# Kernel optimization log

Hardware: AMD Instinct MI355X
Metric: run time of the kernel (lower is better)

The kernel has to match this reference:

```python
import jax, jax.numpy as jnp
import numpy as np

HEADS = 12
D_MODEL = 768
D_TOKEN = D_MODEL // HEADS


def setup_inputs() -> dict:
    key = jax.random.key(0)
    ks = jax.random.split(key, 11)
    B, S, D = 2, 4096, D_MODEL
    scale = 1.0 / np.sqrt(D)
    return {
        "q": jax.random.normal(ks[0], (B, S, D), jnp.float32),
        "k": jax.random.normal(ks[1], (B, S, D), jnp.float32),
        "v": jax.random.normal(ks[2], (B, S, D), jnp.float32),
        "Wq": jax.random.normal(ks[3], (D, D), jnp.float32) * scale,
        "bq": jnp.zeros((D,), jnp.float32),
        "Wk": jax.random.normal(ks[4], (D, D), jnp.float32) * scale,
        "bk": jnp.zeros((D,), jnp.float32),
        "Wv": jax.random.normal(ks[5], (D, D), jnp.float32) * scale,
        "bv": jnp.zeros((D,), jnp.float32),
        "Wo": jax.random.normal(ks[6], (D, D), jnp.float32) * scale,
        "bo": jnp.zeros((D,), jnp.float32),
    }


def reference(q, k, v, Wq, bq, Wk, bk, Wv, bv, Wo, bo):
    B, S, D = q.shape
    H, Dh = HEADS, D_TOKEN
    # Linear projections (torch Linear: x @ W.T + b), split into heads: [B,H,S,Dh]
    qh = (q @ Wq.T + bq).reshape(B, S, H, Dh).transpose(0, 2, 1, 3)
    kh = (k @ Wk.T + bk).reshape(B, S, H, Dh).transpose(0, 2, 1, 3)
    vh = (v @ Wv.T + bv).reshape(B, S, H, Dh).transpose(0, 2, 1, 3)
    # Scaled dot-product attention (full O(S^2) scores, as the original does)
    scores = jnp.einsum("bhqd,bhkd->bhqk", qh, kh) / jnp.sqrt(
        jnp.asarray(Dh, qh.dtype))
    attn = jax.nn.softmax(scores, axis=-1)
    ctx = jnp.einsum("bhqk,bhkd->bhqd", attn, vh)
    ctx = ctx.transpose(0, 2, 1, 3).reshape(B, S, D)
    return ctx @ Wo.T + bo
```

## Files before the change

### kernel.cpp

```cpp
#include <hip/hip_runtime.h>


typedef __attribute__((ext_vector_type(4))) float f32x4;
typedef __attribute__((ext_vector_type(16))) float f32x16;
typedef __attribute__((ext_vector_type(8))) __bf16 bf16x8;
typedef __attribute__((ext_vector_type(2))) int i32x2;
typedef __attribute__((ext_vector_type(4))) unsigned u32x4;
using u16 = unsigned short;
using u32 = unsigned;

__device__ __forceinline__ u16 f2bf(float x) {
  __bf16 h = (__bf16)x;
  return __builtin_bit_cast(u16, h);
}
__device__ __forceinline__ u32 pk2(float lo, float hi) {
  u32 r;
  asm("v_cvt_pk_bf16_f32 %0, %1, %2" : "=v"(r) : "v"(lo), "v"(hi));
  return r;
}
__device__ __forceinline__ void gload16(u16* ldsDst, const u16* gSrc) {
  __builtin_amdgcn_global_load_lds(
      (const __attribute__((address_space(1))) void*)gSrc,
      (__attribute__((address_space(3))) void*)ldsDst, 16, 0, 0);
}
__device__ __forceinline__ f32x4 mfma16(bf16x8 a, bf16x8 b, f32x4 c) {
  return __builtin_amdgcn_mfma_f32_16x16x32_bf16(a, b, c, 0, 0, 0);
}
__device__ __forceinline__ f32x16 mfma32(bf16x8 a, bf16x8 b, f32x16 c) {
  return __builtin_amdgcn_mfma_f32_32x32x16_bf16(a, b, c, 0, 0, 0);
}
__device__ __forceinline__ bf16x8 ld8(const u16* p) { return *(const bf16x8*)p; }

__global__ void cvt_hi(const float4* __restrict__ in0, u16* o0,
                       const float4* __restrict__ in1, u16* o1,
                       const float4* __restrict__ in2, u16* o2,
                       const float4* __restrict__ in3, u16* o3, int n4) {
  const float4* in = in0; u16* o = o0;
  if (blockIdx.y == 1) { in = in1; o = o1; }
  else if (blockIdx.y == 2) { in = in2; o = o2; }
  else if (blockIdx.y == 3) { in = in3; o = o3; }
  const int stride = gridDim.x * blockDim.x;
  for (int i = blockIdx.x * blockDim.x + threadIdx.x; i < n4; i += stride) {
    float4 x = in[i];
    *(ushort4*)&o[i * 4] = make_ushort4(f2bf(x.x), f2bf(x.y), f2bf(x.z), f2bf(x.w));
  }
}

__global__ __launch_bounds__(256, 2) void gemm_qkv(
    const u16* __restrict__ Aq, const u16* __restrict__ Ak, const u16* __restrict__ Av,
    const u16* __restrict__ wq, const u16* __restrict__ wk, const u16* __restrict__ wv,
    const float* __restrict__ bq, const float* __restrict__ bk,
    const float* __restrict__ bv,
    u16* __restrict__ oq, u16* __restrict__ ok, u16* __restrict__ ov,
    float qscale) {
  constexpr int K = 768;
  constexpr int BUF = 8192;
  __shared__ u16 lds[2 * BUF];
  const int z = blockIdx.z;
  const u16* A = (z == 0) ? Aq : (z == 1) ? Ak : Av;
  const u16* Bh = (z == 0) ? wq : (z == 1) ? wk : wv;
  const float* bias = (z == 0) ? bq : (z == 1) ? bk : bv;
  u16* C = (z == 0) ? oq : (z == 1) ? ok : ov;
  const float scale = (z == 0) ? qscale : 1.f;
  const bool vmode = (z == 2);

  const int tid = threadIdx.x, lane = tid & 63, w = tid >> 6;
  const int wr = w >> 1, wc = w & 1;
  const int g = lane >> 4, la = lane & 15;
  const int m0 = blockIdx.x * 128, n0 = blockIdx.y * 128;

  f32x4 acc[4][4] = {};

  auto stage = [&](int buf, int kt) {
    const int k0 = kt * 32;
#pragma unroll
    for (int j = 0; j < 2; ++j) {
      const int t = w * 2 + j;
      const int s = t * 64 + lane;
      const int sr = s >> 3, ph = s & 7, ch = ph ^ (sr & 7);
      const int row = sr * 2 + (ch >> 2), c = ch & 3;
      const int gofs = k0 + c * 8;
      u16* base = &lds[buf * BUF];
      gload16(base + t * 512, A + (size_t)(m0 + row) * K + gofs);
      gload16(base + 4096 + t * 512, Bh + (size_t)(n0 + row) * K + gofs);
    }
  };
  auto rdfrag = [&](const u16* base, int row, int c) -> bf16x8 {
    const int sr = row >> 1;
    const int ph = (((row & 1) << 2) | c) ^ (sr & 7);
    return ld8(base + sr * 64 + ph * 8);
  };

  stage(0, 0);
  __syncthreads();
  constexpr int nk = K / 32;
  int cur = 0;
  for (int kt = 0; kt < nk; ++kt) {
    if (kt + 1 < nk) stage(cur ^ 1, kt + 1);
    const u16* bA = &lds[cur * BUF];
    bf16x8 aH[4], bH[4];
#pragma unroll
    for (int mi = 0; mi < 4; ++mi) aH[mi] = rdfrag(bA, wr * 64 + mi * 16 + la, g);
#pragma unroll
    for (int ni = 0; ni < 4; ++ni) bH[ni] = rdfrag(bA + 4096, wc * 64 + ni * 16 + la, g);
#pragma unroll
    for (int mi = 0; mi < 4; ++mi)
#pragma unroll
      for (int ni = 0; ni < 4; ++ni)
        acc[mi][ni] = mfma16(aH[mi], bH[ni], acc[mi][ni]);
    __syncthreads();
    cur ^= 1;
  }

#pragma unroll
  for (int mi = 0; mi < 4; ++mi) {
    const int mbase = m0 + wr * 64 + mi * 16 + g * 4;
#pragma unroll
    for (int ni = 0; ni < 4; ++ni) {
      const int n = n0 + wc * 64 + ni * 16 + la;
      const float bv_ = bias[n];
#pragma unroll
      for (int r = 0; r < 4; ++r) {
        const int m = mbase + r;
        const float y = (acc[mi][ni][r] + bv_) * scale;
        const int bb = m >> 12, s = m & 4095, hh = n >> 6, dh = n & 63;
        if (!vmode)
          C[((size_t)(bb * 12 + hh) * 4096 + s) * 64 + dh] = f2bf(y);
        else
          C[((size_t)(bb * 12 + hh) * 64 + dh) * 4096 + s] = f2bf(y);
      }
    }
  }
}

__global__ __launch_bounds__(256, 2) void gemm_out(
    const u16* __restrict__ A, const u16* __restrict__ Bh,
    const float* __restrict__ bias, float* __restrict__ Cf) {
  constexpr int K = 768, N = 768;
  constexpr int BUF = 8192;
  __shared__ u16 lds[2 * BUF];
  const int tid = threadIdx.x, lane = tid & 63, w = tid >> 6;
  const int wr = w >> 1, wc = w & 1;
  const int g = lane >> 4, la = lane & 15;
  const int m0 = blockIdx.x * 128, n0 = blockIdx.y * 128;

  f32x4 acc[4][4] = {};

  auto stage = [&](int buf, int kt) {
    const int k0 = kt * 32;
#pragma unroll
    for (int j = 0; j < 2; ++j) {
      const int t = w * 2 + j;
      const int s = t * 64 + lane;
      const int sr = s >> 3, ph = s & 7, ch = ph ^ (sr & 7);
      const int row = sr * 2 + (ch >> 2), c = ch & 3;
      const int gofs = k0 + c * 8;
      u16* base = &lds[buf * BUF];
      gload16(base + t * 512, A + (size_t)(m0 + row) * K + gofs);
      gload16(base + 4096 + t * 512, Bh + (size_t)(n0 + row) * K + gofs);
    }
  };
  auto rdfrag = [&](const u16* base, int row, int c) -> bf16x8 {
    const int sr = row >> 1;
    const int ph = (((row & 1) << 2) | c) ^ (sr & 7);
    return ld8(base + sr * 64 + ph * 8);
  };

  stage(0, 0);
  __syncthreads();
  constexpr int nk = K / 32;
  int cur = 0;
  for (int kt = 0; kt < nk; ++kt) {
    if (kt + 1 < nk) stage(cur ^ 1, kt + 1);
    const u16* bA = &lds[cur * BUF];
    bf16x8 aH[4], bH[4];
#pragma unroll
    for (int mi = 0; mi < 4; ++mi) aH[mi] = rdfrag(bA, wr * 64 + mi * 16 + la, g);
#pragma unroll
    for (int ni = 0; ni < 4; ++ni) bH[ni] = rdfrag(bA + 4096, wc * 64 + ni * 16 + la, g);
#pragma unroll
    for (int mi = 0; mi < 4; ++mi)
#pragma unroll
      for (int ni = 0; ni < 4; ++ni)
        acc[mi][ni] = mfma16(aH[mi], bH[ni], acc[mi][ni]);
    __syncthreads();
    cur ^= 1;
  }

#pragma unroll
  for (int mi = 0; mi < 4; ++mi) {
    const int mbase = m0 + wr * 64 + mi * 16 + g * 4;
#pragma unroll
    for (int ni = 0; ni < 4; ++ni) {
      const int n = n0 + wc * 64 + ni * 16 + la;
      const float bv_ = bias[n];
#pragma unroll
      for (int r = 0; r < 4; ++r)
        Cf[(size_t)(mbase + r) * N + n] = acc[mi][ni][r] + bv_;
    }
  }
}

__global__ __launch_bounds__(256, 3) void flash_attn(
    const u16* __restrict__ Q, const u16* __restrict__ Kt,
    const u16* __restrict__ Vt, u16* __restrict__ ctx) {
  __shared__ u16 lds[2 * 8192];
  const int tid = threadIdx.x, lane = tid & 63, w = tid >> 6;
  const int l5 = lane & 31, hi = lane >> 5;
  const int bh = blockIdx.y, b = bh / 12, h = bh % 12;
  const int q0 = blockIdx.x * 128 + w * 32;
  const size_t kbase = (size_t)bh * 4096 * 64;
  const size_t vbase = (size_t)bh * 64 * 4096;

  bf16x8 aQ[4];
#pragma unroll
  for (int ks = 0; ks < 4; ++ks)
    aQ[ks] = ld8(Q + kbase + (size_t)(q0 + l5) * 64 + ks * 16 + hi * 8);

  f32x16 accO0 = {}, accO1 = {}, accLP = {};
  f32x16 M4;
#pragma unroll
  for (int i = 0; i < 16; ++i) M4[i] = -4.0f;
  const u32x4 onebits = {0x3F803F80u, 0x3F803F80u, 0x3F803F80u, 0x3F803F80u};
  const bf16x8 ones = __builtin_bit_cast(bf16x8, onebits);

  int aK0[4], aK1[4];
  {
    const int r0 = l5, f0 = (r0 & 7) ^ (r0 >> 3);
    const int r1 = 32 + l5, f1 = (r1 & 7) ^ (r1 >> 3);
#pragma unroll
    for (int ks = 0; ks < 4; ++ks) {
      aK0[ks] = r0 * 64 + (((ks * 2 + hi) ^ f0) << 3);
      aK1[ks] = r1 * 64 + (((ks * 2 + hi) ^ f1) << 3);
    }
  }

  const u16 *gk0, *gk1, *gv0, *gv1;
  int dK0, dK1, dV0, dV1;
  {
    const int t0 = w * 2, s0_ = t0 * 64 + lane;
    const int sr0 = s0_ >> 3, c0 = (s0_ & 7) ^ ((sr0 & 7) ^ (sr0 >> 3));
    gk0 = Kt + kbase + (size_t)sr0 * 64 + c0 * 8;
    gv0 = Vt + vbase + (size_t)sr0 * 4096 + c0 * 8;
    dK0 = t0 * 512; dV0 = 4096 + t0 * 512;
    const int t1 = t0 + 1, s1_ = t1 * 64 + lane;
    const int sr1 = s1_ >> 3, c1 = (s1_ & 7) ^ ((sr1 & 7) ^ (sr1 >> 3));
    gk1 = Kt + kbase + (size_t)sr1 * 64 + c1 * 8;
    gv1 = Vt + vbase + (size_t)sr1 * 4096 + c1 * 8;
    dK1 = t1 * 512; dV1 = 4096 + t1 * 512;
  }

  auto stage = [&](int bufbase, int tile) {
    gload16(&lds[bufbase + dK0], gk0 + (size_t)tile * 4096);
    gload16(&lds[bufbase + dK1], gk1 + (size_t)tile * 4096);
    gload16(&lds[bufbase + dV0], gv0 + tile * 64);
    gload16(&lds[bufbase + dV1], gv1 + tile * 64);
  };

  auto body = [&](const int B0) {
    f32x16 s0, s1;
    {
      bf16x8 k0 = ld8(&lds[B0 + aK0[0]]);
      bf16x8 k1 = ld8(&lds[B0 + aK1[0]]);
      s0 = mfma32(k0, aQ[0], M4);
      s1 = mfma32(k1, aQ[0], M4);
    }
#pragma unroll
    for (int ks = 1; ks < 4; ++ks) {
      bf16x8 k0 = ld8(&lds[B0 + aK0[ks]]);
      bf16x8 k1 = ld8(&lds[B0 + aK1[ks]]);
      s0 = mfma32(k0, aQ[ks], s0);
      s1 = mfma32(k1, aQ[ks], s1);
    }
#pragma unroll
    for (int ct = 0; ct < 2; ++ct) {
      const f32x16 sv = ct ? s1 : s0;
      float p[16];
#pragma unroll
      for (int i = 0; i < 16; ++i) p[i] = __builtin_exp2f(sv[i]);
      u32 W[4][2];
#pragma unroll
      for (int qd = 0; qd < 4; ++qd) {
        W[qd][0] = pk2(p[qd * 4 + 0], p[qd * 4 + 1]);
        W[qd][1] = pk2(p[qd * 4 + 2], p[qd * 4 + 3]);
      }
#pragma unroll
      for (int s2 = 0; s2 < 2; ++s2) {
        i32x2 r1 = __builtin_amdgcn_permlane32_swap((int)W[2 * s2][0], (int)W[2 * s2 + 1][0], false, false);
        i32x2 r2 = __builtin_amdgcn_permlane32_swap((int)W[2 * s2][1], (int)W[2 * s2 + 1][1], false, false);
        u32x4 wq = {(u32)r1.x, (u32)r2.x, (u32)r1.y, (u32)r2.y};
        const bf16x8 pb = __builtin_bit_cast(bf16x8, wq);
        const int ksv = ct * 2 + s2;
        bf16x8 v0 = ld8(&lds[B0 + 4096 + aK0[ksv]]);
        bf16x8 v1 = ld8(&lds[B0 + 4096 + aK1[ksv]]);
        accO0 = mfma32(v0, pb, accO0);
        accO1 = mfma32(v1, pb, accO1);
        accLP = mfma32(ones, pb, accLP);
      }
    }
  };

  stage(0, 0);
  __syncthreads();
#pragma unroll 1
  for (int t2 = 0; t2 < 32; ++t2) {
    stage(8192, 2 * t2 + 1);
    body(0);
    __syncthreads();
    if (t2 < 31) stage(0, 2 * t2 + 2);
    body(8192);
    __syncthreads();
  }

  const float inv = __builtin_amdgcn_rcpf(accLP[0]);
  u16* crow = ctx + ((size_t)b * 4096 + q0 + l5) * 768 + h * 64;
#pragma unroll
  for (int dt = 0; dt < 2; ++dt) {
    const f32x16 a = dt ? accO1 : accO0;
#pragma unroll
    for (int rq = 0; rq < 4; ++rq) {
      const int d0 = dt * 32 + 8 * rq + 4 * hi;
      uint2 st;
      st.x = pk2(a[rq * 4 + 0] * inv, a[rq * 4 + 1] * inv);
      st.y = pk2(a[rq * 4 + 2] * inv, a[rq * 4 + 3] * inv);
      *(uint2*)&crow[d0] = st;
    }
  }
}

extern "C" void kernel_launch(void* const* d_in, const int* in_sizes, int n_in,
                              void* d_out, int out_size, void* d_ws, size_t ws_size,
                              hipStream_t stream) {
  constexpr int NQKV = 2 * 4096 * 768;
  constexpr int NW = 768 * 768;
  const float* q = (const float*)d_in[0];
  const float* k = (const float*)d_in[1];
  const float* v = (const float*)d_in[2];
  const float* Wq = (const float*)d_in[3];
  const float* bq = (const float*)d_in[4];
  const float* Wk = (const float*)d_in[5];
  const float* bk = (const float*)d_in[6];
  const float* Wv = (const float*)d_in[7];
  const float* bv = (const float*)d_in[8];
  const float* Wo = (const float*)d_in[9];
  const float* bo = (const float*)d_in[10];

  char* p = (char*)d_ws;
  auto take = [&](size_t n) -> u16* {
    u16* r = (u16*)p;
    p += (n * 2 + 255) & ~(size_t)255;
    return r;
  };
  u16 *q_h = take(NQKV), *k_h = take(NQKV), *v_h = take(NQKV);
  u16 *wq_h = take(NW), *wk_h = take(NW), *wv_h = take(NW), *wo_h = take(NW);
  u16 *qh = take(NQKV), *kh = take(NQKV), *vt = take(NQKV), *ctx = take(NQKV);

  cvt_hi<<<dim3(1024, 3), 256, 0, stream>>>(
      (const float4*)q, q_h, (const float4*)k, k_h, (const float4*)v, v_h,
      nullptr, nullptr, NQKV / 4);
  cvt_hi<<<dim3(288, 4), 256, 0, stream>>>(
      (const float4*)Wq, wq_h, (const float4*)Wk, wk_h,
      (const float4*)Wv, wv_h, (const float4*)Wo, wo_h, NW / 4);

  const float qscale = 0.18033688011112042f;
  gemm_qkv<<<dim3(64, 6, 3), 256, 0, stream>>>(
      q_h, k_h, v_h, wq_h, wk_h, wv_h, bq, bk, bv, qh, kh, vt, qscale);
  flash_attn<<<dim3(32, 24), 256, 0, stream>>>(qh, kh, vt, ctx);
  gemm_out<<<dim3(64, 6), 256, 0, stream>>>(ctx, wo_h, bo, (float*)d_out);
}
```

Measured before the change: 241.6 us.

## Fuse fp32-to-bf16 activation conversion into QKV projection GEMM

Drops the separate conversion kernel for q/k/v. The QKV GEMM now stages fp32 activation tiles straight into LDS with a swizzled layout and packs them to bf16 while reading fragments. This removes a full read and write pass over the three activation tensors and one kernel launch. In exchange the A tile in LDS is twice as large and each fragment read adds conversion instructions. Each fp32 A tile is also reloaded from global memory by all six column blocks.

Result: faster. 230.8 us (-4.4%).

```diff
diff --git a/kernel.cpp b/kernel.cpp
--- a/kernel.cpp
+++ b/kernel.cpp
@@ -47,23 +47,112 @@
 }
 
 __global__ __launch_bounds__(256, 2) void gemm_qkv(
-    const u16* __restrict__ Aq, const u16* __restrict__ Ak, const u16* __restrict__ Av,
+    const float* __restrict__ Aq, const float* __restrict__ Ak,
+    const float* __restrict__ Av,
     const u16* __restrict__ wq, const u16* __restrict__ wk, const u16* __restrict__ wv,
     const float* __restrict__ bq, const float* __restrict__ bk,
     const float* __restrict__ bv,
     u16* __restrict__ oq, u16* __restrict__ ok, u16* __restrict__ ov,
     float qscale) {
   constexpr int K = 768;
-  constexpr int BUF = 8192;
-  __shared__ u16 lds[2 * BUF];
+  constexpr int BUF = 12288;
+  __shared__ __align__(16) u16 lds[2 * BUF];
   const int z = blockIdx.z;
-  const u16* A = (z == 0) ? Aq : (z == 1) ? Ak : Av;
+  const float* A = (z == 0) ? Aq : (z == 1) ? Ak : Av;
   const u16* Bh = (z == 0) ? wq : (z == 1) ? wk : wv;
   const float* bias = (z == 0) ? bq : (z == 1) ? bk : bv;
   u16* C = (z == 0) ? oq : (z == 1) ? ok : ov;
   const float scale = (z == 0) ? qscale : 1.f;
   const bool vmode = (z == 2);
 
+  const int tid = threadIdx.x, lane = tid & 63, w = tid >> 6;
+  const int wr = w >> 1, wc = w & 1;
+  const int g = lane >> 4, la = lane & 15;
+  const int m0 = blockIdx.x * 128, n0 = blockIdx.y * 128;
+
+  f32x4 acc[4][4] = {};
+
+  auto stage = [&](int buf, int kt) {
+    const int k0 = kt * 32;
+    u16* base = &lds[buf * BUF];
+#pragma unroll
+    for (int j = 0; j < 4; ++j) {
+      const int i = w * 4 + j;
+      const int r = i * 8 + (lane >> 3);
+      const int c = (lane & 7) ^ ((lane >> 3) & 7);
+      gload16(base + i * 512, (const u16*)(A + (size_t)(m0 + r) * K + k0 + c * 4));
+    }
+#pragma unroll
+    for (int j = 0; j < 2; ++j) {
+      const int t = w * 2 + j;
+      const int s = t * 64 + lane;
+      const int sr = s >> 3, ph = s & 7, ch = ph ^ (sr & 7);
+      const int row = sr * 2 + (ch >> 2), c = ch & 3;
+      gload16(base + 8192 + t * 512, Bh + (size_t)(n0 + row) * K + k0 + c * 8);
+    }
+  };
+  auto rdfragA = [&](const float* baseF, int row, int gg) -> bf16x8 {
+    const int x = row & 7;
+    const f32x4 u = *(const f32x4*)(baseF + row * 32 + (((2 * gg) ^ x) << 2));
+    const f32x4 v = *(const f32x4*)(baseF + row * 32 + (((2 * gg + 1) ^ x) << 2));
+    u32x4 wq_ = {pk2(u[0], u[1]), pk2(u[2], u[3]), pk2(v[0], v[1]), pk2(v[2], v[3])};
+    return __builtin_bit_cast(bf16x8, wq_);
+  };
+  auto rdfragB = [&](const u16* base, int row, int c) -> bf16x8 {
+    const int sr = row >> 1;
+    const int ph = (((row & 1) << 2) | c) ^ (sr & 7);
+    return ld8(base + sr * 64 + ph * 8);
+  };
+
+  stage(0, 0);
+  __syncthreads();
+  constexpr int nk = K / 32;
+  int cur = 0;
+  for (int kt = 0; kt < nk; ++kt) {
+    if (kt + 1 < nk) stage(cur ^ 1, kt + 1);
+    const float* aF = (const float*)&lds[cur * BUF];
+    const u16* bB = &lds[cur * BUF + 8192];
+    bf16x8 aH[4], bH[4];
+#pragma unroll
+    for (int ni = 0; ni < 4; ++ni) bH[ni] = rdfragB(bB, wc * 64 + ni * 16 + la, g);
+#pragma unroll
+    for (int mi = 0; mi < 4; ++mi) aH[mi] = rdfragA(aF, wr * 64 + mi * 16 + la, g);
+#pragma unroll
+    for (int mi = 0; mi < 4; ++mi)
+#pragma unroll
+      for (int ni = 0; ni < 4; ++ni)
+        acc[mi][ni] = mfma16(aH[mi], bH[ni], acc[mi][ni]);
+    __syncthreads();
+    cur ^= 1;
+  }
+
+#pragma unroll
+  for (int mi = 0; mi < 4; ++mi) {
+    const int mbase = m0 + wr * 64 + mi * 16 + g * 4;
+#pragma unroll
+    for (int ni = 0; ni < 4; ++ni) {
+      const int n = n0 + wc * 64 + ni * 16 + la;
+      const float bv_ = bias[n];
+#pragma unroll
+      for (int r = 0; r < 4; ++r) {
+        const int m = mbase + r;
+        const float y = (acc[mi][ni][r] + bv_) * scale;
+        const int bb = m >> 12, s = m & 4095, hh = n >> 6, dh = n & 63;
+        if (!vmode)
+          C[((size_t)(bb * 12 + hh) * 4096 + s) * 64 + dh] = f2bf(y);
+        else
+          C[((size_t)(bb * 12 + hh) * 64 + dh) * 4096 + s] = f2bf(y);
+      }
+    }
+  }
+}
+
+__global__ __launch_bounds__(256, 2) void gemm_out(
+    const u16* __restrict__ A, const u16* __restrict__ Bh,
+    const float* __restrict__ bias, float* __restrict__ Cf) {
+  constexpr int K = 768, N = 768;
+  constexpr int BUF = 8192;
+  __shared__ __align__(16) u16 lds[2 * BUF];
   const int tid = threadIdx.x, lane = tid & 63, w = tid >> 6;
   const int wr = w >> 1, wc = w & 1;
   const int g = lane >> 4, la = lane & 15;
@@ -120,81 +209,6 @@
       const int n = n0 + wc * 64 + ni * 16 + la;
       const float bv_ = bias[n];
 #pragma unroll
-      for (int r = 0; r < 4; ++r) {
-        const int m = mbase + r;
-        const float y = (acc[mi][ni][r] + bv_) * scale;
-        const int bb = m >> 12, s = m & 4095, hh = n >> 6, dh = n & 63;
-        if (!vmode)
-          C[((size_t)(bb * 12 + hh) * 4096 + s) * 64 + dh] = f2bf(y);
-        else
-          C[((size_t)(bb * 12 + hh) * 64 + dh) * 4096 + s] = f2bf(y);
-      }
-    }
-  }
-}
-
-__global__ __launch_bounds__(256, 2) void gemm_out(
-    const u16* __restrict__ A, const u16* __restrict__ Bh,
-    const float* __restrict__ bias, float* __restrict__ Cf) {
-  constexpr int K = 768, N = 768;
-  constexpr int BUF = 8192;
-  __shared__ u16 lds[2 * BUF];
-  const int tid = threadIdx.x, lane = tid & 63, w = tid >> 6;
-  const int wr = w >> 1, wc = w & 1;
-  const int g = lane >> 4, la = lane & 15;
-  const int m0 = blockIdx.x * 128, n0 = blockIdx.y * 128;
-
-  f32x4 acc[4][4] = {};
-
-  auto stage = [&](int buf, int kt) {
-    const int k0 = kt * 32;
-#pragma unroll
-    for (int j = 0; j < 2; ++j) {
-      const int t = w * 2 + j;
-      const int s = t * 64 + lane;
-      const int sr = s >> 3, ph = s & 7, ch = ph ^ (sr & 7);
-      const int row = sr * 2 + (ch >> 2), c = ch & 3;
-      const int gofs = k0 + c * 8;
-      u16* base = &lds[buf * BUF];
-      gload16(base + t * 512, A + (size_t)(m0 + row) * K + gofs);
-      gload16(base + 4096 + t * 512, Bh + (size_t)(n0 + row) * K + gofs);
-    }
-  };
-  auto rdfrag = [&](const u16* base, int row, int c) -> bf16x8 {
-    const int sr = row >> 1;
-    const int ph = (((row & 1) << 2) | c) ^ (sr & 7);
-    return ld8(base + sr * 64 + ph * 8);
-  };
-
-  stage(0, 0);
-  __syncthreads();
-  constexpr int nk = K / 32;
-  int cur = 0;
-  for (int kt = 0; kt < nk; ++kt) {
-    if (kt + 1 < nk) stage(cur ^ 1, kt + 1);
-    const u16* bA = &lds[cur * BUF];
-    bf16x8 aH[4], bH[4];
-#pragma unroll
-    for (int mi = 0; mi < 4; ++mi) aH[mi] = rdfrag(bA, wr * 64 + mi * 16 + la, g);
-#pragma unroll
-    for (int ni = 0; ni < 4; ++ni) bH[ni] = rdfrag(bA + 4096, wc * 64 + ni * 16 + la, g);
-#pragma unroll
-    for (int mi = 0; mi < 4; ++mi)
-#pragma unroll
-      for (int ni = 0; ni < 4; ++ni)
-        acc[mi][ni] = mfma16(aH[mi], bH[ni], acc[mi][ni]);
-    __syncthreads();
-    cur ^= 1;
-  }
-
-#pragma unroll
-  for (int mi = 0; mi < 4; ++mi) {
-    const int mbase = m0 + wr * 64 + mi * 16 + g * 4;
-#pragma unroll
-    for (int ni = 0; ni < 4; ++ni) {
-      const int n = n0 + wc * 64 + ni * 16 + la;
-      const float bv_ = bias[n];
-#pragma unroll
       for (int r = 0; r < 4; ++r)
         Cf[(size_t)(mbase + r) * N + n] = acc[mi][ni][r] + bv_;
     }
@@ -204,7 +218,7 @@
 __global__ __launch_bounds__(256, 3) void flash_attn(
     const u16* __restrict__ Q, const u16* __restrict__ Kt,
     const u16* __restrict__ Vt, u16* __restrict__ ctx) {
-  __shared__ u16 lds[2 * 8192];
+  __shared__ __align__(16) u16 lds[2 * 8192];
   const int tid = threadIdx.x, lane = tid & 63, w = tid >> 6;
   const int l5 = lane & 31, hi = lane >> 5;
   const int bh = blockIdx.y, b = bh / 12, h = bh % 12;
@@ -351,20 +365,16 @@
     p += (n * 2 + 255) & ~(size_t)255;
     return r;
   };
-  u16 *q_h = take(NQKV), *k_h = take(NQKV), *v_h = take(NQKV);
   u16 *wq_h = take(NW), *wk_h = take(NW), *wv_h = take(NW), *wo_h = take(NW);
   u16 *qh = take(NQKV), *kh = take(NQKV), *vt = take(NQKV), *ctx = take(NQKV);
 
-  cvt_hi<<<dim3(1024, 3), 256, 0, stream>>>(
-      (const float4*)q, q_h, (const float4*)k, k_h, (const float4*)v, v_h,
-      nullptr, nullptr, NQKV / 4);
   cvt_hi<<<dim3(288, 4), 256, 0, stream>>>(
       (const float4*)Wq, wq_h, (const float4*)Wk, wk_h,
       (const float4*)Wv, wv_h, (const float4*)Wo, wo_h, NW / 4);
 
   const float qscale = 0.18033688011112042f;
   gemm_qkv<<<dim3(64, 6, 3), 256, 0, stream>>>(
-      q_h, k_h, v_h, wq_h, wk_h, wv_h, bq, bk, bv, qh, kh, vt, qscale);
+      q, k, v, wq_h, wk_h, wv_h, bq, bk, bv, qh, kh, vt, qscale);
   flash_attn<<<dim3(32, 24), 256, 0, stream>>>(qh, kh, vt, ctx);
   gemm_out<<<dim3(64, 6), 256, 0, stream>>>(ctx, wo_h, bo, (float*)d_out);
 }
```
